# Kernel optimization log

Hardware: AMD Instinct MI355X
Metric: run time of the kernel (lower is better)

The kernel has to match this reference:

```python
import jax, jax.numpy as jnp
import numpy as np

N_NODES = 10000
N_EDGES = 320000
CH = 64          # multiplicity per irrep (64x0e node feats)
R_DIM = 8        # radial embedding dim
L_MAX = 2
N_L = L_MAX + 1
SH_DIM = 9       # 1 + 3 + 5
AVG_NEIGH = 32.0
MLP_HID = 64


def setup_inputs() -> dict:
    key = jax.random.key(0)
    ks = jax.random.split(key, 11)
    return {
        "edge_vectors": jax.random.normal(ks[0], (N_EDGES, 3), jnp.float32),
        "node_feats": jax.random.normal(ks[1], (N_NODES, CH), jnp.float32),
        "radial_embeddings": jax.random.normal(ks[2], (N_EDGES, R_DIM), jnp.float32),
        "senders": jax.random.randint(ks[3], (N_EDGES,), 0, N_NODES),
        "receivers": jax.random.randint(ks[4], (N_EDGES,), 0, N_NODES),
        # learned params (e3nn Linear / MLP weights, unit normal init)
        "W_up": jax.random.normal(ks[5], (CH, CH), jnp.float32),
        "W_mlp1": jax.random.normal(ks[6], (R_DIM, MLP_HID), jnp.float32),
        "W_mlp2": jax.random.normal(ks[7], (MLP_HID, MLP_HID), jnp.float32),
        "W_mlp3": jax.random.normal(ks[8], (MLP_HID, MLP_HID), jnp.float32),
        "W_mlp4": jax.random.normal(ks[9], (MLP_HID, N_L * CH), jnp.float32),
        "W_down": jax.random.normal(ks[10], (N_L, CH, CH), jnp.float32),
    }


def spherical_harmonics(vec):
    """Component-normalized real spherical harmonics (||Y_l||^2 = 2l+1), l=0..2,
    on normalized edge vectors (e3nn normalize=True, normalization='component')."""
    v = vec / jnp.linalg.norm(vec, axis=-1, keepdims=True)
    x, y, z = v[..., 0], v[..., 1], v[..., 2]
    c15 = float(np.sqrt(15.0))
    c5 = float(np.sqrt(5.0))
    sh2 = jnp.stack(
        [c15 * x * y, c15 * y * z, 0.5 * c5 * (3.0 * z * z - 1.0),
         c15 * x * z, 0.5 * c15 * (x * x - y * y)], axis=-1)
    return jnp.concatenate(
        [jnp.ones_like(x)[..., None], float(np.sqrt(3.0)) * v, sh2], axis=-1)  # [E, 9]


def reference(edge_vectors, node_feats, radial_embeddings, senders, receivers,
              W_up, W_mlp1, W_mlp2, W_mlp3, W_mlp4, W_down):
    inv_ch = 1.0 / np.sqrt(CH)
    n_nodes = node_feats.shape[0]

    # linear_up: scalar irreps -> plain channel mixing with e3nn 1/sqrt(fan_in)
    h = (node_feats @ W_up) * inv_ch                               # [N, CH]

    sh = spherical_harmonics(edge_vectors)                         # [E, 9]

    # radial MLP -> one weight per (channel, l) tensor-product path
    m = radial_embeddings
    for W in (W_mlp1, W_mlp2, W_mlp3):
        m = jax.nn.silu((m @ W) / np.sqrt(W.shape[0]))
    mix = (m @ W_mlp4) / np.sqrt(MLP_HID)                          # [E, N_L*CH]
    w = mix.reshape(-1, N_L, CH).transpose(0, 2, 1)                # [E, CH, N_L]
    # broadcast each per-irrep weight over its 2l+1 components
    w = jnp.repeat(w, np.array([1, 3, 5]), axis=-1,
                   total_repeat_length=SH_DIM)                     # [E, CH, 9]

    # tensor product (scalar node feats x Y_l) with radial weights: messages
    msg = h[senders][:, :, None] * sh[:, None, :] * w              # [E, CH, 9]

    # scatter-add to receivers, normalize by avg_num_neighbors
    agg = jax.ops.segment_sum(msg.reshape(msg.shape[0], -1),
                              receivers, num_segments=n_nodes)
    agg = (agg / AVG_NEIGH).reshape(n_nodes, CH, SH_DIM)           # [N, CH, 9]

    # linear_down: independent channel mixing per l (equivariant Linear)
    outs = []
    start = 0
    for l in range(N_L):
        d = 2 * l + 1
        o = jnp.einsum('ncm,cd->ndm', agg[:, :, start:start + d], W_down[l]) * inv_ch
        outs.append(o.reshape(n_nodes, -1))
        start += d
    return jnp.concatenate(outs, axis=-1)                          # [N, 576]
```

## Files before the change

kernel.cpp:

```cpp
#include <hip/hip_runtime.h>
#include <hip/hip_bf16.h>
#include <math.h>

#define N_NODES 10000
#define N_EDGES 320000
#define CH 64
#define MIXW 192
#define EREC 12

#define W1_OFF 0
#define W2_OFF 512
#define W3_OFF 5120
#define W4_OFF 9728
#define W_TOT 23552
#define ACT_STRIDE 72

#define EPB 128

#define PREP_BLKS 92
#define H_BLKS 625
#define HIST_BLKS 1250

typedef __attribute__((ext_vector_type(8))) short bf16x8;
typedef __attribute__((ext_vector_type(4))) float f32x4;
#define MFMA16(a, b, c) __builtin_amdgcn_mfma_f32_16x16x32_bf16(a, b, c, 0, 0, 0)

__device__ __forceinline__ float bf2f(unsigned short u) {
    union { unsigned int i; float f; } v; v.i = ((unsigned int)u) << 16; return v.f;
}
__device__ __forceinline__ unsigned short f2bf(float f) {
    __hip_bfloat16 b = __float2bfloat16(f);
    return *reinterpret_cast<unsigned short*>(&b);
}
__device__ __forceinline__ float silu(float t) {
    return t * __builtin_amdgcn_rcpf(1.0f + __expf(-t));
}

__device__ __forceinline__ void load_bfrag(bf16x8 (&b)[4][2],
                                           const unsigned short* __restrict__ wbase,
                                           int lrow, int quad) {
#pragma unroll
    for (int nt = 0; nt < 4; ++nt)
#pragma unroll
        for (int kh = 0; kh < 2; ++kh)
            b[nt][kh] = *(const bf16x8*)(wbase + (nt * 16 + lrow) * 72 + kh * 32 + quad * 8);
}

__device__ __forceinline__ void layer64(unsigned short* act, const bf16x8 (&b)[4][2],
                                        int em0, int em1, int cr0, int cr1,
                                        int lrow, int quad) {
    bf16x8 a00 = *(const bf16x8*)(act + em0 * ACT_STRIDE + quad * 8);
    bf16x8 a01 = *(const bf16x8*)(act + em0 * ACT_STRIDE + 32 + quad * 8);
    bf16x8 a10 = *(const bf16x8*)(act + em1 * ACT_STRIDE + quad * 8);
    bf16x8 a11 = *(const bf16x8*)(act + em1 * ACT_STRIDE + 32 + quad * 8);
#pragma unroll
    for (int nt = 0; nt < 4; ++nt) {
        f32x4 c0 = {0.f, 0.f, 0.f, 0.f};
        f32x4 c1 = {0.f, 0.f, 0.f, 0.f};
        c0 = MFMA16(a00, b[nt][0], c0);
        c0 = MFMA16(a01, b[nt][1], c0);
        c1 = MFMA16(a10, b[nt][0], c1);
        c1 = MFMA16(a11, b[nt][1], c1);
#pragma unroll
        for (int r = 0; r < 4; ++r) {
            act[(cr0 + r) * ACT_STRIDE + nt * 16 + lrow] = f2bf(silu(c0[r]));
            act[(cr1 + r) * ACT_STRIDE + nt * 16 + lrow] = f2bf(silu(c1[r]));
        }
    }
}

__device__ __forceinline__ void l4_third(unsigned short* act,
                                         const int (&pj)[4],
                                         unsigned short* __restrict__ hw,
                                         const bf16x8 (&b)[4][2],
                                         const bf16x8& a00, const bf16x8& a01,
                                         const bf16x8& a10, const bf16x8& a11,
                                         const float (&hreg0)[4][4],
                                         const float (&hreg1)[4][4],
                                         int T, int cr0, int cr1, int wr0,
                                         int lane, int lrow, int quad) {
#pragma unroll
    for (int ntl = 0; ntl < 4; ++ntl) {
        f32x4 c0 = {0.f, 0.f, 0.f, 0.f};
        f32x4 c1 = {0.f, 0.f, 0.f, 0.f};
        c0 = MFMA16(a00, b[ntl][0], c0);
        c0 = MFMA16(a01, b[ntl][1], c0);
        c1 = MFMA16(a10, b[ntl][0], c1);
        c1 = MFMA16(a11, b[ntl][1], c1);
#pragma unroll
        for (int r = 0; r < 4; ++r) {
            act[(cr0 + r) * ACT_STRIDE + ntl * 16 + lrow] = f2bf(c0[r] * hreg0[r][ntl]);
            act[(cr1 + r) * ACT_STRIDE + ntl * 16 + lrow] = f2bf(c1[r] * hreg1[r][ntl]);
        }
    }
#pragma unroll
    for (int j = 0; j < 4; ++j) {
        int idx = lane + 64 * j;
        int row = idx >> 3, c8 = idx & 7;
        uint4 v = *(const uint4*)(act + (wr0 + row) * ACT_STRIDE + c8 * 8);
        *(uint4*)(hw + (size_t)pj[j] * MIXW + T * 64 + c8 * 8) = v;
    }
}

__global__ __launch_bounds__(256) void k_pre(const float* __restrict__ W1,
                                             const float* __restrict__ W2,
                                             const float* __restrict__ W3,
                                             const float* __restrict__ W4,
                                             unsigned short* __restrict__ wimg,
                                             const float* __restrict__ nf,
                                             const float* __restrict__ Wup,
                                             float* __restrict__ h,
                                             const int* __restrict__ recv,
                                             int* __restrict__ counts) {
    int bid = blockIdx.x;
    int t = threadIdx.x;
    if (bid < PREP_BLKS) {
        int i = bid * 256 + t;
        if (i >= W_TOT) return;
        float v;
        if (i < W2_OFF) {
            int n = i >> 3, k = i & 7;
            v = W1[k * 64 + n] * 0.35355339059327376f;
        } else if (i < W3_OFF) {
            int j = i - W2_OFF; int n = j / 72, k = j % 72;
            v = (k < 64) ? W2[k * 64 + n] * 0.125f : 0.f;
        } else if (i < W4_OFF) {
            int j = i - W3_OFF; int n = j / 72, k = j % 72;
            v = (k < 64) ? W3[k * 64 + n] * 0.125f : 0.f;
        } else {
            int j = i - W4_OFF; int n = j / 72, k = j % 72;
            v = (k < 64) ? W4[k * MIXW + n] : 0.f;
        }
        wimg[i] = f2bf(v);
    } else if (bid < PREP_BLKS + H_BLKS) {
        int nb = __builtin_amdgcn_readfirstlane(
            (bid - PREP_BLKS) * 16 + (t >> 6) * 4);
        int lane = t & 63;
        const float* nrow = nf + (size_t)nb * CH;
        float a0 = 0.f, a1 = 0.f, a2 = 0.f, a3 = 0.f;
#pragma unroll
        for (int k = 0; k < CH; ++k) {
            float w = Wup[k * CH + lane];
            a0 = fmaf(nrow[k], w, a0);
            a1 = fmaf(nrow[CH + k], w, a1);
            a2 = fmaf(nrow[2 * CH + k], w, a2);
            a3 = fmaf(nrow[3 * CH + k], w, a3);
        }
        h[(size_t)nb * CH + lane] = a0 * 0.015625f;
        h[(size_t)(nb + 1) * CH + lane] = a1 * 0.015625f;
        h[(size_t)(nb + 2) * CH + lane] = a2 * 0.015625f;
        h[(size_t)(nb + 3) * CH + lane] = a3 * 0.015625f;
    } else {
        int e = (bid - PREP_BLKS - H_BLKS) * 256 + t;
        atomicAdd(&counts[recv[e]], 1);
    }
}

__global__ __launch_bounds__(1024) void k_scan(const int* __restrict__ counts,
                                               int* __restrict__ offsets,
                                               int* __restrict__ cursor) {
    __shared__ int wsum[16];
    int t = threadIdx.x;
    const int CHUNK = 10;
    int base = t * CHUNK;
    int s = 0;
    for (int i = 0; i < CHUNK; ++i) {
        int idx = base + i;
        if (idx < N_NODES) s += counts[idx];
    }
    int lane = t & 63, wv = t >> 6;
    int x = s;
#pragma unroll
    for (int off = 1; off < 64; off <<= 1) {
        int y = __shfl_up(x, off, 64);
        if (lane >= off) x += y;
    }
    if (lane == 63) wsum[wv] = x;
    __syncthreads();
    if (wv == 0 && lane < 16) {
        int v = wsum[lane];
#pragma unroll
        for (int off = 1; off < 16; off <<= 1) {
            int y = __shfl_up(v, off, 64);
            if (lane >= off) v += y;
        }
        wsum[lane] = v;
    }
    __syncthreads();
    int wbase = (wv == 0) ? 0 : wsum[wv - 1];
    int run = wbase + x - s;
    for (int i = 0; i < CHUNK; ++i) {
        int idx = base + i;
        if (idx < N_NODES) {
            offsets[idx] = run;
            cursor[idx] = run;
            run += counts[idx];
        }
    }
    if (t == 1023) offsets[N_NODES] = wbase + x;
}

__global__ __launch_bounds__(256) void k_mlp(const float* __restrict__ ev,
                                             const float* __restrict__ rad,
                                             const unsigned short* __restrict__ wimg,
                                             const int* __restrict__ senders,
                                             const int* __restrict__ recv,
                                             int* __restrict__ cursor,
                                             const float* __restrict__ h,
                                             unsigned short* __restrict__ hw,
                                             float* __restrict__ erec) {
    __shared__ unsigned short act[EPB * ACT_STRIDE];
    __shared__ int s_pos[EPB];
    __shared__ int s_snd[EPB];

    const int t = threadIdx.x;
    const int e0 = blockIdx.x * EPB;
    const int wv = t >> 6;
    const int lane = t & 63;
    const int lrow = lane & 15;
    const int quad = lane >> 4;
    const int wr0 = wv * 32;
    const int em0 = wr0 + lrow;
    const int em1 = em0 + 16;
    const int cr0 = wr0 + quad * 4;
    const int cr1 = cr0 + 16;

    bf16x8 ar0 = {0, 0, 0, 0, 0, 0, 0, 0};
    bf16x8 ar1 = {0, 0, 0, 0, 0, 0, 0, 0};
    bf16x8 bw1[4];
#pragma unroll
    for (int nt = 0; nt < 4; ++nt) bw1[nt] = (bf16x8){0, 0, 0, 0, 0, 0, 0, 0};
    if (quad == 0) {
        const float4* rp0 = (const float4*)(rad + (size_t)(e0 + em0) * 8);
        const float4* rp1 = (const float4*)(rad + (size_t)(e0 + em1) * 8);
        float4 u = rp0[0], v = rp0[1];
        ar0[0] = (short)f2bf(u.x); ar0[1] = (short)f2bf(u.y);
        ar0[2] = (short)f2bf(u.z); ar0[3] = (short)f2bf(u.w);
        ar0[4] = (short)f2bf(v.x); ar0[5] = (short)f2bf(v.y);
        ar0[6] = (short)f2bf(v.z); ar0[7] = (short)f2bf(v.w);
        u = rp1[0]; v = rp1[1];
        ar1[0] = (short)f2bf(u.x); ar1[1] = (short)f2bf(u.y);
        ar1[2] = (short)f2bf(u.z); ar1[3] = (short)f2bf(u.w);
        ar1[4] = (short)f2bf(v.x); ar1[5] = (short)f2bf(v.y);
        ar1[6] = (short)f2bf(v.z); ar1[7] = (short)f2bf(v.w);
#pragma unroll
        for (int nt = 0; nt < 4; ++nt)
            bw1[nt] = *(const bf16x8*)(wimg + W1_OFF + (nt * 16 + lrow) * 8);
    }
    bf16x8 bA[4][2], bB[4][2];
    load_bfrag(bA, wimg + W2_OFF, lrow, quad);

    if (lane < 32) {
        int e = e0 + wr0 + lane;
        int p = atomicAdd(&cursor[recv[e]], 1);
        s_pos[wr0 + lane] = p;
        s_snd[wr0 + lane] = senders[e];
        float vx = ev[(size_t)e * 3 + 0], vy = ev[(size_t)e * 3 + 1], vz = ev[(size_t)e * 3 + 2];
        float inv = rsqrtf(vx * vx + vy * vy + vz * vz);
        float x = vx * inv, y = vy * inv, z = vz * inv;
        const float s3 = 1.7320508075688772f;
        const float s15 = 3.872983346207417f;
        const float s5 = 2.2360679774997896f;
        float4* rp = (float4*)(erec + (size_t)p * EREC);
        rp[0] = make_float4(1.0f, s3 * x, s3 * y, s3 * z);
        rp[1] = make_float4(s15 * x * y, s15 * y * z, 0.5f * s5 * (3.0f * z * z - 1.0f), s15 * x * z);
        rp[2] = make_float4(0.5f * s15 * (x * x - y * y), 0.f, 0.f, 0.f);
    }

#pragma unroll
    for (int nt = 0; nt < 4; ++nt) {
        f32x4 c0 = {0.f, 0.f, 0.f, 0.f};
        f32x4 c1 = {0.f, 0.f, 0.f, 0.f};
        c0 = MFMA16(ar0, bw1[nt], c0);
        c1 = MFMA16(ar1, bw1[nt], c1);
#pragma unroll
        for (int r = 0; r < 4; ++r) {
            act[(cr0 + r) * ACT_STRIDE + nt * 16 + lrow] = f2bf(silu(c0[r]));
            act[(cr1 + r) * ACT_STRIDE + nt * 16 + lrow] = f2bf(silu(c1[r]));
        }
    }

    load_bfrag(bB, wimg + W3_OFF, lrow, quad);
    layer64(act, bA, em0, em1, cr0, cr1, lrow, quad);

    load_bfrag(bA, wimg + W4_OFF, lrow, quad);
    int sn0[4], sn1[4];
#pragma unroll
    for (int r = 0; r < 4; ++r) {
        sn0[r] = s_snd[cr0 + r];
        sn1[r] = s_snd[cr1 + r];
    }
    layer64(act, bB, em0, em1, cr0, cr1, lrow, quad);

    float hreg0[4][4], hreg1[4][4];
#pragma unroll
    for (int r = 0; r < 4; ++r) {
        const float* hb0 = h + (size_t)sn0[r] * CH + lrow;
        const float* hb1 = h + (size_t)sn1[r] * CH + lrow;
#pragma unroll
        for (int ntl = 0; ntl < 4; ++ntl) {
            hreg0[r][ntl] = hb0[ntl * 16];
            hreg1[r][ntl] = hb1[ntl * 16];
        }
    }

    {
        bf16x8 a00 = *(const bf16x8*)(act + em0 * ACT_STRIDE + quad * 8);
        bf16x8 a01 = *(const bf16x8*)(act + em0 * ACT_STRIDE + 32 + quad * 8);
        bf16x8 a10 = *(const bf16x8*)(act + em1 * ACT_STRIDE + quad * 8);
        bf16x8 a11 = *(const bf16x8*)(act + em1 * ACT_STRIDE + 32 + quad * 8);
        int pj[4];
#pragma unroll
        for (int j = 0; j < 4; ++j) pj[j] = s_pos[wr0 + ((lane + 64 * j) >> 3)];

        load_bfrag(bB, wimg + W4_OFF + 64 * 72, lrow, quad);
        l4_third(act, pj, hw, bA, a00, a01, a10, a11, hreg0, hreg1,
                 0, cr0, cr1, wr0, lane, lrow, quad);
        load_bfrag(bA, wimg + W4_OFF + 2 * 64 * 72, lrow, quad);
        l4_third(act, pj, hw, bB, a00, a01, a10, a11, hreg0, hreg1,
                 1, cr0, cr1, wr0, lane, lrow, quad);
        l4_third(act, pj, hw, bA, a00, a01, a10, a11, hreg0, hreg1,
                 2, cr0, cr1, wr0, lane, lrow, quad);
    }
}

__global__ __launch_bounds__(256, 4) void k_aggdown(const int* __restrict__ offsets,
                                                    const float* __restrict__ erec,
                                                    const unsigned short* __restrict__ hw,
                                                    const float* __restrict__ Wd,
                                                    float* __restrict__ out) {
    __shared__ float sg[4][576];
    int wv = threadIdx.x >> 6;
    int lane = threadIdx.x & 63;
    int node = __builtin_amdgcn_readfirstlane(blockIdx.x * 4 + wv);
    int s0 = __builtin_amdgcn_readfirstlane(offsets[node]);
    int s1 = __builtin_amdgcn_readfirstlane(offsets[node + 1]);
    float acc[9] = {0.f, 0.f, 0.f, 0.f, 0.f, 0.f, 0.f, 0.f, 0.f};
#pragma unroll 8
    for (int i = s0; i < s1; ++i) {
        const float* rp = erec + (size_t)i * EREC;
        const unsigned short* hrow = hw + (size_t)i * MIXW;
        float w0 = bf2f(hrow[lane]);
        float w1 = bf2f(hrow[64 + lane]);
        float w2 = bf2f(hrow[128 + lane]);
        acc[0] += w0 * rp[0];
        acc[1] += w1 * rp[1];
        acc[2] += w1 * rp[2];
        acc[3] += w1 * rp[3];
        acc[4] += w2 * rp[4];
        acc[5] += w2 * rp[5];
        acc[6] += w2 * rp[6];
        acc[7] += w2 * rp[7];
        acc[8] += w2 * rp[8];
    }
    float* arow = sg[wv];
#pragma unroll
    for (int m = 0; m < 9; ++m) arow[lane * 9 + m] = acc[m] * (1.0f / 32.0f);

    float* orow = out + (size_t)node * 576;
    {
        float a = 0.f;
#pragma unroll
        for (int c = 0; c < 64; ++c) a += arow[c * 9] * Wd[c * 64 + lane];
        orow[lane] = a * 0.125f;
    }
    {
        float m3[3] = {0.f, 0.f, 0.f};
#pragma unroll
        for (int c = 0; c < 64; ++c) {
            float w = Wd[(64 + c) * 64 + lane];
#pragma unroll
            for (int mm = 0; mm < 3; ++mm) m3[mm] += arow[c * 9 + 1 + mm] * w;
        }
#pragma unroll
        for (int mm = 0; mm < 3; ++mm) orow[64 + lane * 3 + mm] = m3[mm] * 0.125f;
    }
    {
        float m5[5] = {0.f, 0.f, 0.f, 0.f, 0.f};
#pragma unroll
        for (int c = 0; c < 64; ++c) {
            float w = Wd[(128 + c) * 64 + lane];
#pragma unroll
            for (int mm = 0; mm < 5; ++mm) m5[mm] += arow[c * 9 + 4 + mm] * w;
        }
#pragma unroll
        for (int mm = 0; mm < 5; ++mm) orow[256 + lane * 5 + mm] = m5[mm] * 0.125f;
    }
}

static inline size_t align256(size_t x) { return (x + 255) & ~(size_t)255; }

extern "C" void kernel_launch(void* const* d_in, const int* in_sizes, int n_in,
                              void* d_out, int out_size, void* d_ws, size_t ws_size,
                              hipStream_t stream) {
    const float* edge_vectors = (const float*)d_in[0];
    const float* node_feats   = (const float*)d_in[1];
    const float* radial       = (const float*)d_in[2];
    const int*   senders      = (const int*)d_in[3];
    const int*   receivers    = (const int*)d_in[4];
    const float* W_up         = (const float*)d_in[5];
    const float* W_mlp1       = (const float*)d_in[6];
    const float* W_mlp2       = (const float*)d_in[7];
    const float* W_mlp3       = (const float*)d_in[8];
    const float* W_mlp4       = (const float*)d_in[9];
    const float* W_down       = (const float*)d_in[10];
    float* out = (float*)d_out;

    char* base = (char*)d_ws;
    size_t off = 0;
    float* h = (float*)(base + off);              off = align256(off + (size_t)N_NODES * CH * 4);
    unsigned short* hw = (unsigned short*)(base + off); off = align256(off + (size_t)N_EDGES * MIXW * 2);
    float* erec = (float*)(base + off);           off = align256(off + (size_t)N_EDGES * EREC * 4);
    unsigned short* wimg = (unsigned short*)(base + off); off = align256(off + (size_t)W_TOT * 2);
    int* counts = (int*)(base + off);             off = align256(off + (size_t)N_NODES * 4);
    int* offsets = (int*)(base + off);            off = align256(off + (size_t)(N_NODES + 1) * 4);
    int* cursor = (int*)(base + off);             off = align256(off + (size_t)N_NODES * 4);

    hipMemsetAsync(counts, 0, (size_t)N_NODES * 4, stream);

    k_pre<<<PREP_BLKS + H_BLKS + HIST_BLKS, 256, 0, stream>>>(
        W_mlp1, W_mlp2, W_mlp3, W_mlp4, wimg, node_feats, W_up, h, receivers, counts);
    k_scan<<<1, 1024, 0, stream>>>(counts, offsets, cursor);
    k_mlp<<<N_EDGES / EPB, 256, 0, stream>>>(edge_vectors, radial, wimg, senders,
                                             receivers, cursor, h, hw, erec);
    k_aggdown<<<N_NODES / 4, 256, 0, stream>>>(offsets, erec, hw, W_down, out);
}
```

Before: 206.6 us.

## Move sender-feature multiply into aggregation and double edges per MLP block

The gather of h[sender] and its multiply move out of the edge MLP kernel and into the aggregation kernel. The sender index is stored in a spare slot of the per-edge record, and the scale factors are rebalanced between W4 and h so the result is unchanged. The MLP kernel now handles 256 edges per block, with each wave processing four 16-row tiles instead of two. This is meant to cut register pressure and gather latency in the MLP kernel and to amortize weight-fragment loads. The cost is an extra random gather of h per edge inside the aggregation loop.

```diff
diff --git a/kernel.cpp b/kernel.cpp
--- a/kernel.cpp
+++ b/kernel.cpp
@@ -15,7 +15,7 @@
 #define W_TOT 23552
 #define ACT_STRIDE 72
 
-#define EPB 128
+#define EPB 256
 
 #define PREP_BLKS 92
 #define H_BLKS 625
@@ -46,59 +46,61 @@
             b[nt][kh] = *(const bf16x8*)(wbase + (nt * 16 + lrow) * 72 + kh * 32 + quad * 8);
 }
 
-__device__ __forceinline__ void layer64(unsigned short* act, const bf16x8 (&b)[4][2],
-                                        int em0, int em1, int cr0, int cr1,
-                                        int lrow, int quad) {
-    bf16x8 a00 = *(const bf16x8*)(act + em0 * ACT_STRIDE + quad * 8);
-    bf16x8 a01 = *(const bf16x8*)(act + em0 * ACT_STRIDE + 32 + quad * 8);
-    bf16x8 a10 = *(const bf16x8*)(act + em1 * ACT_STRIDE + quad * 8);
-    bf16x8 a11 = *(const bf16x8*)(act + em1 * ACT_STRIDE + 32 + quad * 8);
+__device__ __forceinline__ void layer64_t4(unsigned short* act, const bf16x8 (&b)[4][2],
+                                           const int (&em)[4], const int (&cr)[4],
+                                           int lrow, int quad) {
+    bf16x8 a[4][2];
+#pragma unroll
+    for (int t = 0; t < 4; ++t) {
+        a[t][0] = *(const bf16x8*)(act + em[t] * ACT_STRIDE + quad * 8);
+        a[t][1] = *(const bf16x8*)(act + em[t] * ACT_STRIDE + 32 + quad * 8);
+    }
 #pragma unroll
     for (int nt = 0; nt < 4; ++nt) {
-        f32x4 c0 = {0.f, 0.f, 0.f, 0.f};
-        f32x4 c1 = {0.f, 0.f, 0.f, 0.f};
-        c0 = MFMA16(a00, b[nt][0], c0);
-        c0 = MFMA16(a01, b[nt][1], c0);
-        c1 = MFMA16(a10, b[nt][0], c1);
-        c1 = MFMA16(a11, b[nt][1], c1);
-#pragma unroll
-        for (int r = 0; r < 4; ++r) {
-            act[(cr0 + r) * ACT_STRIDE + nt * 16 + lrow] = f2bf(silu(c0[r]));
-            act[(cr1 + r) * ACT_STRIDE + nt * 16 + lrow] = f2bf(silu(c1[r]));
-        }
-    }
-}
-
-__device__ __forceinline__ void l4_third(unsigned short* act,
-                                         const int (&pj)[4],
-                                         unsigned short* __restrict__ hw,
-                                         const bf16x8 (&b)[4][2],
-                                         const bf16x8& a00, const bf16x8& a01,
-                                         const bf16x8& a10, const bf16x8& a11,
-                                         const float (&hreg0)[4][4],
-                                         const float (&hreg1)[4][4],
-                                         int T, int cr0, int cr1, int wr0,
-                                         int lane, int lrow, int quad) {
-#pragma unroll
-    for (int ntl = 0; ntl < 4; ++ntl) {
-        f32x4 c0 = {0.f, 0.f, 0.f, 0.f};
-        f32x4 c1 = {0.f, 0.f, 0.f, 0.f};
-        c0 = MFMA16(a00, b[ntl][0], c0);
-        c0 = MFMA16(a01, b[ntl][1], c0);
-        c1 = MFMA16(a10, b[ntl][0], c1);
-        c1 = MFMA16(a11, b[ntl][1], c1);
-#pragma unroll
-        for (int r = 0; r < 4; ++r) {
-            act[(cr0 + r) * ACT_STRIDE + ntl * 16 + lrow] = f2bf(c0[r] * hreg0[r][ntl]);
-            act[(cr1 + r) * ACT_STRIDE + ntl * 16 + lrow] = f2bf(c1[r] * hreg1[r][ntl]);
-        }
-    }
-#pragma unroll
-    for (int j = 0; j < 4; ++j) {
+        f32x4 c[4];
+#pragma unroll
+        for (int t = 0; t < 4; ++t) {
+            c[t] = (f32x4){0.f, 0.f, 0.f, 0.f};
+            c[t] = MFMA16(a[t][0], b[nt][0], c[t]);
+            c[t] = MFMA16(a[t][1], b[nt][1], c[t]);
+        }
+#pragma unroll
+        for (int t = 0; t < 4; ++t)
+#pragma unroll
+            for (int r = 0; r < 4; ++r)
+                act[(cr[t] + r) * ACT_STRIDE + nt * 16 + lrow] = f2bf(silu(c[t][r]));
+    }
+}
+
+__device__ __forceinline__ void l4_third_t4(unsigned short* act,
+                                            const int* s_pos,
+                                            unsigned short* __restrict__ hw,
+                                            const bf16x8 (&b)[4][2],
+                                            const bf16x8 (&a)[4][2],
+                                            const int (&cr)[4],
+                                            int T, int wr0, int lane, int lrow, int quad) {
+#pragma unroll
+    for (int nt = 0; nt < 4; ++nt) {
+        f32x4 c[4];
+#pragma unroll
+        for (int t = 0; t < 4; ++t) {
+            c[t] = (f32x4){0.f, 0.f, 0.f, 0.f};
+            c[t] = MFMA16(a[t][0], b[nt][0], c[t]);
+            c[t] = MFMA16(a[t][1], b[nt][1], c[t]);
+        }
+#pragma unroll
+        for (int t = 0; t < 4; ++t)
+#pragma unroll
+            for (int r = 0; r < 4; ++r)
+                act[(cr[t] + r) * ACT_STRIDE + nt * 16 + lrow] = f2bf(c[t][r]);
+    }
+#pragma unroll
+    for (int j = 0; j < 8; ++j) {
         int idx = lane + 64 * j;
         int row = idx >> 3, c8 = idx & 7;
+        int p = s_pos[wr0 + row];
         uint4 v = *(const uint4*)(act + (wr0 + row) * ACT_STRIDE + c8 * 8);
-        *(uint4*)(hw + (size_t)pj[j] * MIXW + T * 64 + c8 * 8) = v;
+        *(uint4*)(hw + (size_t)p * MIXW + T * 64 + c8 * 8) = v;
     }
 }
 
@@ -129,7 +131,7 @@
             v = (k < 64) ? W3[k * 64 + n] * 0.125f : 0.f;
         } else {
             int j = i - W4_OFF; int n = j / 72, k = j % 72;
-            v = (k < 64) ? W4[k * MIXW + n] : 0.f;
+            v = (k < 64) ? W4[k * MIXW + n] * 0.125f : 0.f;
         }
         wimg[i] = f2bf(v);
     } else if (bid < PREP_BLKS + H_BLKS) {
@@ -146,10 +148,10 @@
             a2 = fmaf(nrow[2 * CH + k], w, a2);
             a3 = fmaf(nrow[3 * CH + k], w, a3);
         }
-        h[(size_t)nb * CH + lane] = a0 * 0.015625f;
-        h[(size_t)(nb + 1) * CH + lane] = a1 * 0.015625f;
-        h[(size_t)(nb + 2) * CH + lane] = a2 * 0.015625f;
-        h[(size_t)(nb + 3) * CH + lane] = a3 * 0.015625f;
+        h[(size_t)nb * CH + lane] = a0 * 0.125f;
+        h[(size_t)(nb + 1) * CH + lane] = a1 * 0.125f;
+        h[(size_t)(nb + 2) * CH + lane] = a2 * 0.125f;
+        h[(size_t)(nb + 3) * CH + lane] = a3 * 0.125f;
     } else {
         int e = (bid - PREP_BLKS - H_BLKS) * 256 + t;
         atomicAdd(&counts[recv[e]], 1);
@@ -206,12 +208,10 @@
                                              const int* __restrict__ senders,
                                              const int* __restrict__ recv,
                                              int* __restrict__ cursor,
-                                             const float* __restrict__ h,
                                              unsigned short* __restrict__ hw,
                                              float* __restrict__ erec) {
     __shared__ unsigned short act[EPB * ACT_STRIDE];
     __shared__ int s_pos[EPB];
-    __shared__ int s_snd[EPB];
 
     const int t = threadIdx.x;
     const int e0 = blockIdx.x * EPB;
@@ -219,42 +219,43 @@
     const int lane = t & 63;
     const int lrow = lane & 15;
     const int quad = lane >> 4;
-    const int wr0 = wv * 32;
-    const int em0 = wr0 + lrow;
-    const int em1 = em0 + 16;
-    const int cr0 = wr0 + quad * 4;
-    const int cr1 = cr0 + 16;
-
-    bf16x8 ar0 = {0, 0, 0, 0, 0, 0, 0, 0};
-    bf16x8 ar1 = {0, 0, 0, 0, 0, 0, 0, 0};
+    const int wr0 = wv * 64;
+    int em[4], cr[4];
+#pragma unroll
+    for (int tt = 0; tt < 4; ++tt) {
+        em[tt] = wr0 + tt * 16 + lrow;
+        cr[tt] = wr0 + tt * 16 + quad * 4;
+    }
+
+    bf16x8 ar[4];
     bf16x8 bw1[4];
 #pragma unroll
-    for (int nt = 0; nt < 4; ++nt) bw1[nt] = (bf16x8){0, 0, 0, 0, 0, 0, 0, 0};
+    for (int nt = 0; nt < 4; ++nt) {
+        ar[nt] = (bf16x8){0, 0, 0, 0, 0, 0, 0, 0};
+        bw1[nt] = (bf16x8){0, 0, 0, 0, 0, 0, 0, 0};
+    }
+    bf16x8 bA[4][2], bB[4][2];
+    load_bfrag(bA, wimg + W2_OFF, lrow, quad);
     if (quad == 0) {
-        const float4* rp0 = (const float4*)(rad + (size_t)(e0 + em0) * 8);
-        const float4* rp1 = (const float4*)(rad + (size_t)(e0 + em1) * 8);
-        float4 u = rp0[0], v = rp0[1];
-        ar0[0] = (short)f2bf(u.x); ar0[1] = (short)f2bf(u.y);
-        ar0[2] = (short)f2bf(u.z); ar0[3] = (short)f2bf(u.w);
-        ar0[4] = (short)f2bf(v.x); ar0[5] = (short)f2bf(v.y);
-        ar0[6] = (short)f2bf(v.z); ar0[7] = (short)f2bf(v.w);
-        u = rp1[0]; v = rp1[1];
-        ar1[0] = (short)f2bf(u.x); ar1[1] = (short)f2bf(u.y);
-        ar1[2] = (short)f2bf(u.z); ar1[3] = (short)f2bf(u.w);
-        ar1[4] = (short)f2bf(v.x); ar1[5] = (short)f2bf(v.y);
-        ar1[6] = (short)f2bf(v.z); ar1[7] = (short)f2bf(v.w);
+#pragma unroll
+        for (int tt = 0; tt < 4; ++tt) {
+            const float4* rp0 = (const float4*)(rad + (size_t)(e0 + em[tt]) * 8);
+            float4 u = rp0[0], v = rp0[1];
+            ar[tt][0] = (short)f2bf(u.x); ar[tt][1] = (short)f2bf(u.y);
+            ar[tt][2] = (short)f2bf(u.z); ar[tt][3] = (short)f2bf(u.w);
+            ar[tt][4] = (short)f2bf(v.x); ar[tt][5] = (short)f2bf(v.y);
+            ar[tt][6] = (short)f2bf(v.z); ar[tt][7] = (short)f2bf(v.w);
+        }
 #pragma unroll
         for (int nt = 0; nt < 4; ++nt)
             bw1[nt] = *(const bf16x8*)(wimg + W1_OFF + (nt * 16 + lrow) * 8);
     }
-    bf16x8 bA[4][2], bB[4][2];
-    load_bfrag(bA, wimg + W2_OFF, lrow, quad);
-
-    if (lane < 32) {
+
+    {
         int e = e0 + wr0 + lane;
         int p = atomicAdd(&cursor[recv[e]], 1);
         s_pos[wr0 + lane] = p;
-        s_snd[wr0 + lane] = senders[e];
+        int snd = senders[e];
         float vx = ev[(size_t)e * 3 + 0], vy = ev[(size_t)e * 3 + 1], vz = ev[(size_t)e * 3 + 2];
         float inv = rsqrtf(vx * vx + vy * vy + vz * vz);
         float x = vx * inv, y = vy * inv, z = vz * inv;
@@ -264,69 +265,49 @@
         float4* rp = (float4*)(erec + (size_t)p * EREC);
         rp[0] = make_float4(1.0f, s3 * x, s3 * y, s3 * z);
         rp[1] = make_float4(s15 * x * y, s15 * y * z, 0.5f * s5 * (3.0f * z * z - 1.0f), s15 * x * z);
-        rp[2] = make_float4(0.5f * s15 * (x * x - y * y), 0.f, 0.f, 0.f);
+        rp[2] = make_float4(0.5f * s15 * (x * x - y * y), __int_as_float(snd), 0.f, 0.f);
     }
 
 #pragma unroll
     for (int nt = 0; nt < 4; ++nt) {
-        f32x4 c0 = {0.f, 0.f, 0.f, 0.f};
-        f32x4 c1 = {0.f, 0.f, 0.f, 0.f};
-        c0 = MFMA16(ar0, bw1[nt], c0);
-        c1 = MFMA16(ar1, bw1[nt], c1);
-#pragma unroll
-        for (int r = 0; r < 4; ++r) {
-            act[(cr0 + r) * ACT_STRIDE + nt * 16 + lrow] = f2bf(silu(c0[r]));
-            act[(cr1 + r) * ACT_STRIDE + nt * 16 + lrow] = f2bf(silu(c1[r]));
-        }
+        f32x4 c[4];
+#pragma unroll
+        for (int tt = 0; tt < 4; ++tt) {
+            c[tt] = (f32x4){0.f, 0.f, 0.f, 0.f};
+            c[tt] = MFMA16(ar[tt], bw1[nt], c[tt]);
+        }
+#pragma unroll
+        for (int tt = 0; tt < 4; ++tt)
+#pragma unroll
+            for (int r = 0; r < 4; ++r)
+                act[(cr[tt] + r) * ACT_STRIDE + nt * 16 + lrow] = f2bf(silu(c[tt][r]));
     }
 
     load_bfrag(bB, wimg + W3_OFF, lrow, quad);
-    layer64(act, bA, em0, em1, cr0, cr1, lrow, quad);
+    layer64_t4(act, bA, em, cr, lrow, quad);
 
     load_bfrag(bA, wimg + W4_OFF, lrow, quad);
-    int sn0[4], sn1[4];
-#pragma unroll
-    for (int r = 0; r < 4; ++r) {
-        sn0[r] = s_snd[cr0 + r];
-        sn1[r] = s_snd[cr1 + r];
-    }
-    layer64(act, bB, em0, em1, cr0, cr1, lrow, quad);
-
-    float hreg0[4][4], hreg1[4][4];
-#pragma unroll
-    for (int r = 0; r < 4; ++r) {
-        const float* hb0 = h + (size_t)sn0[r] * CH + lrow;
-        const float* hb1 = h + (size_t)sn1[r] * CH + lrow;
-#pragma unroll
-        for (int ntl = 0; ntl < 4; ++ntl) {
-            hreg0[r][ntl] = hb0[ntl * 16];
-            hreg1[r][ntl] = hb1[ntl * 16];
-        }
-    }
+    layer64_t4(act, bB, em, cr, lrow, quad);
 
     {
-        bf16x8 a00 = *(const bf16x8*)(act + em0 * ACT_STRIDE + quad * 8);
-        bf16x8 a01 = *(const bf16x8*)(act + em0 * ACT_STRIDE + 32 + quad * 8);
-        bf16x8 a10 = *(const bf16x8*)(act + em1 * ACT_STRIDE + quad * 8);
-        bf16x8 a11 = *(const bf16x8*)(act + em1 * ACT_STRIDE + 32 + quad * 8);
-        int pj[4];
-#pragma unroll
-        for (int j = 0; j < 4; ++j) pj[j] = s_pos[wr0 + ((lane + 64 * j) >> 3)];
-
+        bf16x8 a[4][2];
+#pragma unroll
+        for (int tt = 0; tt < 4; ++tt) {
+            a[tt][0] = *(const bf16x8*)(act + em[tt] * ACT_STRIDE + quad * 8);
+            a[tt][1] = *(const bf16x8*)(act + em[tt] * ACT_STRIDE + 32 + quad * 8);
+        }
         load_bfrag(bB, wimg + W4_OFF + 64 * 72, lrow, quad);
-        l4_third(act, pj, hw, bA, a00, a01, a10, a11, hreg0, hreg1,
-                 0, cr0, cr1, wr0, lane, lrow, quad);
+        l4_third_t4(act, s_pos, hw, bA, a, cr, 0, wr0, lane, lrow, quad);
         load_bfrag(bA, wimg + W4_OFF + 2 * 64 * 72, lrow, quad);
-        l4_third(act, pj, hw, bB, a00, a01, a10, a11, hreg0, hreg1,
-                 1, cr0, cr1, wr0, lane, lrow, quad);
-        l4_third(act, pj, hw, bA, a00, a01, a10, a11, hreg0, hreg1,
-                 2, cr0, cr1, wr0, lane, lrow, quad);
+        l4_third_t4(act, s_pos, hw, bB, a, cr, 1, wr0, lane, lrow, quad);
+        l4_third_t4(act, s_pos, hw, bA, a, cr, 2, wr0, lane, lrow, quad);
     }
 }
 
 __global__ __launch_bounds__(256, 4) void k_aggdown(const int* __restrict__ offsets,
                                                     const float* __restrict__ erec,
                                                     const unsigned short* __restrict__ hw,
+                                                    const float* __restrict__ h,
                                                     const float* __restrict__ Wd,
                                                     float* __restrict__ out) {
     __shared__ float sg[4][576];
@@ -336,13 +317,15 @@
     int s0 = __builtin_amdgcn_readfirstlane(offsets[node]);
     int s1 = __builtin_amdgcn_readfirstlane(offsets[node + 1]);
     float acc[9] = {0.f, 0.f, 0.f, 0.f, 0.f, 0.f, 0.f, 0.f, 0.f};
-#pragma unroll 8
+#pragma unroll 4
     for (int i = s0; i < s1; ++i) {
         const float* rp = erec + (size_t)i * EREC;
         const unsigned short* hrow = hw + (size_t)i * MIXW;
-        float w0 = bf2f(hrow[lane]);
-        float w1 = bf2f(hrow[64 + lane]);
-        float w2 = bf2f(hrow[128 + lane]);
+        int snd = __float_as_int(rp[9]);
+        float hh = h[(size_t)snd * CH + lane];
+        float w0 = bf2f(hrow[lane]) * hh;
+        float w1 = bf2f(hrow[64 + lane]) * hh;
+        float w2 = bf2f(hrow[128 + lane]) * hh;
         acc[0] += w0 * rp[0];
         acc[1] += w1 * rp[1];
         acc[2] += w1 * rp[2];
@@ -422,6 +405,6 @@
         W_mlp1, W_mlp2, W_mlp3, W_mlp4, wimg, node_feats, W_up, h, receivers, counts);
     k_scan<<<1, 1024, 0, stream>>>(counts, offsets, cursor);
     k_mlp<<<N_EDGES / EPB, 256, 0, stream>>>(edge_vectors, radial, wimg, senders,
-                                             receivers, cursor, h, hw, erec);
-    k_aggdown<<<N_NODES / 4, 256, 0, stream>>>(offsets, erec, hw, W_down, out);
-}
+                                             receivers, cursor, hw, erec);
+    k_aggdown<<<N_NODES / 4, 256, 0, stream>>>(offsets, erec, hw, h, W_down, out);
+}
```

Result: slower. 219.3 us (+6.2%).

## Replace CSR sort-and-gather aggregation with direct atomic scatter into node buffer

Applied to the files above, without the earlier changes.

Drops the receiver histogram, scan and per-edge hw/erec intermediates. The MLP kernel now scales its output by spherical harmonics and atomically adds into a zeroed per-node fp32 buffer, which the down-projection kernel reads directly. This removes a large per-edge write and read round trip and two launches. In exchange it issues many fp32 global atomics to random receivers and makes summation order nondeterministic.

```diff
diff --git a/kernel.cpp b/kernel.cpp
--- a/kernel.cpp
+++ b/kernel.cpp
@@ -6,7 +6,8 @@
 #define N_EDGES 320000
 #define CH 64
 #define MIXW 192
-#define EREC 12
+#define AGG_STRIDE 576
+#define SH_STRIDE 9
 
 #define W1_OFF 0
 #define W2_OFF 512
@@ -19,7 +20,6 @@
 
 #define PREP_BLKS 92
 #define H_BLKS 625
-#define HIST_BLKS 1250
 
 typedef __attribute__((ext_vector_type(8))) short bf16x8;
 typedef __attribute__((ext_vector_type(4))) float f32x4;
@@ -69,16 +69,17 @@
     }
 }
 
-__device__ __forceinline__ void l4_third(unsigned short* act,
-                                         const int (&pj)[4],
-                                         unsigned short* __restrict__ hw,
-                                         const bf16x8 (&b)[4][2],
-                                         const bf16x8& a00, const bf16x8& a01,
-                                         const bf16x8& a10, const bf16x8& a11,
-                                         const float (&hreg0)[4][4],
-                                         const float (&hreg1)[4][4],
-                                         int T, int cr0, int cr1, int wr0,
-                                         int lane, int lrow, int quad) {
+__device__ __forceinline__ void l4_third_agg(unsigned short* act,
+                                             const int* s_rcv,
+                                             const float* s_sh,
+                                             float* __restrict__ agg,
+                                             const bf16x8 (&b)[4][2],
+                                             const bf16x8& a00, const bf16x8& a01,
+                                             const bf16x8& a10, const bf16x8& a11,
+                                             const float (&hreg0)[4][4],
+                                             const float (&hreg1)[4][4],
+                                             int T, int cr0, int cr1, int wr0,
+                                             int lane, int lrow, int quad) {
 #pragma unroll
     for (int ntl = 0; ntl < 4; ++ntl) {
         f32x4 c0 = {0.f, 0.f, 0.f, 0.f};
@@ -93,12 +94,26 @@
             act[(cr1 + r) * ACT_STRIDE + ntl * 16 + lrow] = f2bf(c1[r] * hreg1[r][ntl]);
         }
     }
-#pragma unroll
-    for (int j = 0; j < 4; ++j) {
-        int idx = lane + 64 * j;
-        int row = idx >> 3, c8 = idx & 7;
-        uint4 v = *(const uint4*)(act + (wr0 + row) * ACT_STRIDE + c8 * 8);
-        *(uint4*)(hw + (size_t)pj[j] * MIXW + T * 64 + c8 * 8) = v;
+#pragma unroll 8
+    for (int r = 0; r < 32; ++r) {
+        int row = wr0 + r;
+        int node = __builtin_amdgcn_readfirstlane(s_rcv[row]);
+        float w = bf2f(act[row * ACT_STRIDE + lane]);
+        float* ab = agg + (size_t)node * AGG_STRIDE + lane;
+        const float* shr = s_sh + row * SH_STRIDE;
+        if (T == 0) {
+            atomicAdd(ab, w);
+        } else if (T == 1) {
+            atomicAdd(ab + 64, w * shr[1]);
+            atomicAdd(ab + 128, w * shr[2]);
+            atomicAdd(ab + 192, w * shr[3]);
+        } else {
+            atomicAdd(ab + 256, w * shr[4]);
+            atomicAdd(ab + 320, w * shr[5]);
+            atomicAdd(ab + 384, w * shr[6]);
+            atomicAdd(ab + 448, w * shr[7]);
+            atomicAdd(ab + 512, w * shr[8]);
+        }
     }
 }
 
@@ -109,9 +124,7 @@
                                              unsigned short* __restrict__ wimg,
                                              const float* __restrict__ nf,
                                              const float* __restrict__ Wup,
-                                             float* __restrict__ h,
-                                             const int* __restrict__ recv,
-                                             int* __restrict__ counts) {
+                                             float* __restrict__ h) {
     int bid = blockIdx.x;
     int t = threadIdx.x;
     if (bid < PREP_BLKS) {
@@ -132,7 +145,7 @@
             v = (k < 64) ? W4[k * MIXW + n] : 0.f;
         }
         wimg[i] = f2bf(v);
-    } else if (bid < PREP_BLKS + H_BLKS) {
+    } else {
         int nb = __builtin_amdgcn_readfirstlane(
             (bid - PREP_BLKS) * 16 + (t >> 6) * 4);
         int lane = t & 63;
@@ -150,54 +163,7 @@
         h[(size_t)(nb + 1) * CH + lane] = a1 * 0.015625f;
         h[(size_t)(nb + 2) * CH + lane] = a2 * 0.015625f;
         h[(size_t)(nb + 3) * CH + lane] = a3 * 0.015625f;
-    } else {
-        int e = (bid - PREP_BLKS - H_BLKS) * 256 + t;
-        atomicAdd(&counts[recv[e]], 1);
-    }
-}
-
-__global__ __launch_bounds__(1024) void k_scan(const int* __restrict__ counts,
-                                               int* __restrict__ offsets,
-                                               int* __restrict__ cursor) {
-    __shared__ int wsum[16];
-    int t = threadIdx.x;
-    const int CHUNK = 10;
-    int base = t * CHUNK;
-    int s = 0;
-    for (int i = 0; i < CHUNK; ++i) {
-        int idx = base + i;
-        if (idx < N_NODES) s += counts[idx];
-    }
-    int lane = t & 63, wv = t >> 6;
-    int x = s;
-#pragma unroll
-    for (int off = 1; off < 64; off <<= 1) {
-        int y = __shfl_up(x, off, 64);
-        if (lane >= off) x += y;
-    }
-    if (lane == 63) wsum[wv] = x;
-    __syncthreads();
-    if (wv == 0 && lane < 16) {
-        int v = wsum[lane];
-#pragma unroll
-        for (int off = 1; off < 16; off <<= 1) {
-            int y = __shfl_up(v, off, 64);
-            if (lane >= off) v += y;
-        }
-        wsum[lane] = v;
-    }
-    __syncthreads();
-    int wbase = (wv == 0) ? 0 : wsum[wv - 1];
-    int run = wbase + x - s;
-    for (int i = 0; i < CHUNK; ++i) {
-        int idx = base + i;
-        if (idx < N_NODES) {
-            offsets[idx] = run;
-            cursor[idx] = run;
-            run += counts[idx];
-        }
-    }
-    if (t == 1023) offsets[N_NODES] = wbase + x;
+    }
 }
 
 __global__ __launch_bounds__(256) void k_mlp(const float* __restrict__ ev,
@@ -205,13 +171,12 @@
                                              const unsigned short* __restrict__ wimg,
                                              const int* __restrict__ senders,
                                              const int* __restrict__ recv,
-                                             int* __restrict__ cursor,
                                              const float* __restrict__ h,
-                                             unsigned short* __restrict__ hw,
-                                             float* __restrict__ erec) {
+                                             float* __restrict__ agg) {
     __shared__ unsigned short act[EPB * ACT_STRIDE];
-    __shared__ int s_pos[EPB];
+    __shared__ int s_rcv[EPB];
     __shared__ int s_snd[EPB];
+    __shared__ float s_sh[EPB * SH_STRIDE];
 
     const int t = threadIdx.x;
     const int e0 = blockIdx.x * EPB;
@@ -251,20 +216,26 @@
     load_bfrag(bA, wimg + W2_OFF, lrow, quad);
 
     if (lane < 32) {
-        int e = e0 + wr0 + lane;
-        int p = atomicAdd(&cursor[recv[e]], 1);
-        s_pos[wr0 + lane] = p;
-        s_snd[wr0 + lane] = senders[e];
+        int row = wr0 + lane;
+        int e = e0 + row;
+        s_rcv[row] = recv[e];
+        s_snd[row] = senders[e];
         float vx = ev[(size_t)e * 3 + 0], vy = ev[(size_t)e * 3 + 1], vz = ev[(size_t)e * 3 + 2];
         float inv = rsqrtf(vx * vx + vy * vy + vz * vz);
         float x = vx * inv, y = vy * inv, z = vz * inv;
         const float s3 = 1.7320508075688772f;
         const float s15 = 3.872983346207417f;
         const float s5 = 2.2360679774997896f;
-        float4* rp = (float4*)(erec + (size_t)p * EREC);
-        rp[0] = make_float4(1.0f, s3 * x, s3 * y, s3 * z);
-        rp[1] = make_float4(s15 * x * y, s15 * y * z, 0.5f * s5 * (3.0f * z * z - 1.0f), s15 * x * z);
-        rp[2] = make_float4(0.5f * s15 * (x * x - y * y), 0.f, 0.f, 0.f);
+        float* shr = s_sh + row * SH_STRIDE;
+        shr[0] = 1.0f;
+        shr[1] = s3 * x;
+        shr[2] = s3 * y;
+        shr[3] = s3 * z;
+        shr[4] = s15 * x * y;
+        shr[5] = s15 * y * z;
+        shr[6] = 0.5f * s5 * (3.0f * z * z - 1.0f);
+        shr[7] = s15 * x * z;
+        shr[8] = 0.5f * s15 * (x * x - y * y);
     }
 
 #pragma unroll
@@ -309,53 +280,29 @@
         bf16x8 a01 = *(const bf16x8*)(act + em0 * ACT_STRIDE + 32 + quad * 8);
         bf16x8 a10 = *(const bf16x8*)(act + em1 * ACT_STRIDE + quad * 8);
         bf16x8 a11 = *(const bf16x8*)(act + em1 * ACT_STRIDE + 32 + quad * 8);
-        int pj[4];
-#pragma unroll
-        for (int j = 0; j < 4; ++j) pj[j] = s_pos[wr0 + ((lane + 64 * j) >> 3)];
 
         load_bfrag(bB, wimg + W4_OFF + 64 * 72, lrow, quad);
-        l4_third(act, pj, hw, bA, a00, a01, a10, a11, hreg0, hreg1,
-                 0, cr0, cr1, wr0, lane, lrow, quad);
+        l4_third_agg(act, s_rcv, s_sh, agg, bA, a00, a01, a10, a11, hreg0, hreg1,
+                     0, cr0, cr1, wr0, lane, lrow, quad);
         load_bfrag(bA, wimg + W4_OFF + 2 * 64 * 72, lrow, quad);
-        l4_third(act, pj, hw, bB, a00, a01, a10, a11, hreg0, hreg1,
-                 1, cr0, cr1, wr0, lane, lrow, quad);
-        l4_third(act, pj, hw, bA, a00, a01, a10, a11, hreg0, hreg1,
-                 2, cr0, cr1, wr0, lane, lrow, quad);
-    }
-}
-
-__global__ __launch_bounds__(256, 4) void k_aggdown(const int* __restrict__ offsets,
-                                                    const float* __restrict__ erec,
-                                                    const unsigned short* __restrict__ hw,
-                                                    const float* __restrict__ Wd,
-                                                    float* __restrict__ out) {
+        l4_third_agg(act, s_rcv, s_sh, agg, bB, a00, a01, a10, a11, hreg0, hreg1,
+                     1, cr0, cr1, wr0, lane, lrow, quad);
+        l4_third_agg(act, s_rcv, s_sh, agg, bA, a00, a01, a10, a11, hreg0, hreg1,
+                     2, cr0, cr1, wr0, lane, lrow, quad);
+    }
+}
+
+__global__ __launch_bounds__(256, 4) void k_down(const float* __restrict__ agg,
+                                                 const float* __restrict__ Wd,
+                                                 float* __restrict__ out) {
     __shared__ float sg[4][576];
     int wv = threadIdx.x >> 6;
     int lane = threadIdx.x & 63;
     int node = __builtin_amdgcn_readfirstlane(blockIdx.x * 4 + wv);
-    int s0 = __builtin_amdgcn_readfirstlane(offsets[node]);
-    int s1 = __builtin_amdgcn_readfirstlane(offsets[node + 1]);
-    float acc[9] = {0.f, 0.f, 0.f, 0.f, 0.f, 0.f, 0.f, 0.f, 0.f};
-#pragma unroll 8
-    for (int i = s0; i < s1; ++i) {
-        const float* rp = erec + (size_t)i * EREC;
-        const unsigned short* hrow = hw + (size_t)i * MIXW;
-        float w0 = bf2f(hrow[lane]);
-        float w1 = bf2f(hrow[64 + lane]);
-        float w2 = bf2f(hrow[128 + lane]);
-        acc[0] += w0 * rp[0];
-        acc[1] += w1 * rp[1];
-        acc[2] += w1 * rp[2];
-        acc[3] += w1 * rp[3];
-        acc[4] += w2 * rp[4];
-        acc[5] += w2 * rp[5];
-        acc[6] += w2 * rp[6];
-        acc[7] += w2 * rp[7];
-        acc[8] += w2 * rp[8];
-    }
+    const float* ag = agg + (size_t)node * AGG_STRIDE + lane;
     float* arow = sg[wv];
 #pragma unroll
-    for (int m = 0; m < 9; ++m) arow[lane * 9 + m] = acc[m] * (1.0f / 32.0f);
+    for (int m = 0; m < 9; ++m) arow[lane * 9 + m] = ag[m * 64] * (1.0f / 32.0f);
 
     float* orow = out + (size_t)node * 576;
     {
@@ -409,19 +356,14 @@
     char* base = (char*)d_ws;
     size_t off = 0;
     float* h = (float*)(base + off);              off = align256(off + (size_t)N_NODES * CH * 4);
-    unsigned short* hw = (unsigned short*)(base + off); off = align256(off + (size_t)N_EDGES * MIXW * 2);
-    float* erec = (float*)(base + off);           off = align256(off + (size_t)N_EDGES * EREC * 4);
+    float* agg = (float*)(base + off);            off = align256(off + (size_t)N_NODES * AGG_STRIDE * 4);
     unsigned short* wimg = (unsigned short*)(base + off); off = align256(off + (size_t)W_TOT * 2);
-    int* counts = (int*)(base + off);             off = align256(off + (size_t)N_NODES * 4);
-    int* offsets = (int*)(base + off);            off = align256(off + (size_t)(N_NODES + 1) * 4);
-    int* cursor = (int*)(base + off);             off = align256(off + (size_t)N_NODES * 4);
-
-    hipMemsetAsync(counts, 0, (size_t)N_NODES * 4, stream);
-
-    k_pre<<<PREP_BLKS + H_BLKS + HIST_BLKS, 256, 0, stream>>>(
-        W_mlp1, W_mlp2, W_mlp3, W_mlp4, wimg, node_feats, W_up, h, receivers, counts);
-    k_scan<<<1, 1024, 0, stream>>>(counts, offsets, cursor);
+
+    hipMemsetAsync(agg, 0, (size_t)N_NODES * AGG_STRIDE * 4, stream);
+
+    k_pre<<<PREP_BLKS + H_BLKS, 256, 0, stream>>>(
+        W_mlp1, W_mlp2, W_mlp3, W_mlp4, wimg, node_feats, W_up, h);
     k_mlp<<<N_EDGES / EPB, 256, 0, stream>>>(edge_vectors, radial, wimg, senders,
-                                             receivers, cursor, h, hw, erec);
-    k_aggdown<<<N_NODES / 4, 256, 0, stream>>>(offsets, erec, hw, W_down, out);
-}
+                                             receivers, h, agg);
+    k_down<<<N_NODES / 4, 256, 0, stream>>>(agg, W_down, out);
+}
```

New measurement: 693.7 us. 236% more time.
